# Performance work log

Hardware: AMD Instinct MI355X
Metric: run time of the kernel (lower is better)

The kernel has to match this reference:

```python
import jax, jax.numpy as jnp
import numpy as np

B, T, C, H = 2, 2048, 1024, 16
D = C // H  # head_dim = 64

def setup_inputs() -> dict:
    key = jax.random.key(0)
    k1, k2, k3, k4, k5 = jax.random.split(key, 5)
    x = jax.random.normal(k1, (B, T, C), dtype=jnp.float32)
    # RoPE tables (realistic frequencies)
    inv_freq = 1.0 / (10000.0 ** (jnp.arange(0, D // 2, dtype=jnp.float32) / (D // 2)))
    pos = jnp.arange(T, dtype=jnp.float32)
    ang = pos[:, None] * inv_freq[None, :]          # (T, D/2)
    cos, sin = jnp.cos(ang), jnp.sin(ang)
    # causal mask (True = keep)
    mask = jnp.tril(jnp.ones((T, T), dtype=bool))
    W_qkv = jax.random.normal(k2, (3 * C, C), dtype=jnp.float32) * (1.0 / np.sqrt(C))
    W_out = jax.random.normal(k3, (C, C), dtype=jnp.float32) * (1.0 / np.sqrt(C))
    return {"x": x, "cos": cos, "sin": sin, "mask": mask, "W_qkv": W_qkv, "W_out": W_out}

def apply_rope(x, cos, sin):
    # x: (B, H, T, D); cos/sin: (T, D/2)
    d = x.shape[-1] // 2
    x1, x2 = x[..., :d], x[..., d:]
    c = cos[None, None, :x.shape[2], :]
    s = sin[None, None, :x.shape[2], :]
    return jnp.concatenate([x1 * c - x2 * s, x2 * c + x1 * s], axis=-1)

def reference(x, cos, sin, mask, W_qkv, W_out):
    b, t, c = x.shape
    qkv = (x @ W_qkv.T).reshape(b, t, 3, H, D)
    q, k, v = qkv[:, :, 0], qkv[:, :, 1], qkv[:, :, 2]   # (b, t, H, D)
    q = q.transpose(0, 2, 1, 3)
    k = k.transpose(0, 2, 1, 3)
    v = v.transpose(0, 2, 1, 3)                           # (b, H, t, D)
    q = apply_rope(q, cos, sin)
    k = apply_rope(k, cos, sin)
    attn = jnp.einsum('bhqd,bhkd->bhqk', q, k) / jnp.sqrt(jnp.asarray(D, x.dtype))
    attn = jnp.where(mask[None, None, :, :], attn, -jnp.inf)
    attn = jax.nn.softmax(attn, axis=-1)
    out = jnp.einsum('bhqk,bhkd->bhqd', attn, v)          # (b, H, t, D)
    out = out.transpose(0, 2, 1, 3).reshape(b, t, c)
    return out @ W_out.T
```

## Files before the change

### kernel.cpp

```cpp
#include <hip/hip_runtime.h>
#include <stdint.h>

typedef __bf16 bf16;
typedef __bf16 bf16x4 __attribute__((ext_vector_type(4)));
typedef __bf16 bf16x8 __attribute__((ext_vector_type(8)));
typedef float f32x4 __attribute__((ext_vector_type(4)));

#define TSEQ 2048
#define NHEAD 16
#define HDIM 64
#define CDIM 1024

#define AS1(p) ((const __attribute__((address_space(1))) void*)(p))
#define AS3(p) ((__attribute__((address_space(3))) void*)(p))

#if __has_builtin(__builtin_amdgcn_exp2f)
#define EXP2(x) __builtin_amdgcn_exp2f(x)
#else
#define EXP2(x) exp2f(x)
#endif

__global__ __launch_bounds__(256) void cast3_bf16(const float* __restrict__ in1, int n1,
                                                  const float* __restrict__ in2, int n2,
                                                  const float* __restrict__ in3, int n3,
                                                  bf16* __restrict__ out1,
                                                  bf16* __restrict__ out2,
                                                  bf16* __restrict__ out3) {
  int i = (blockIdx.x * 256 + threadIdx.x) * 8;
  const float* src;
  bf16* dst;
  if (i < n1) {
    src = in1 + i; dst = out1 + i;
  } else if (i < n1 + n2) {
    src = in2 + (i - n1); dst = out2 + (i - n1);
  } else if (i < n1 + n2 + n3) {
    src = in3 + (i - n1 - n2); dst = out3 + (i - n1 - n2);
  } else {
    return;
  }
  float4 a = *(const float4*)src;
  float4 b = *(const float4*)(src + 4);
  bf16x8 r;
  r[0] = (bf16)a.x; r[1] = (bf16)a.y; r[2] = (bf16)a.z; r[3] = (bf16)a.w;
  r[4] = (bf16)b.x; r[5] = (bf16)b.y; r[6] = (bf16)b.z; r[7] = (bf16)b.w;
  *(bf16x8*)dst = r;
}

__global__ __launch_bounds__(256) void gemm_qkv_rope(const bf16* __restrict__ A,
                                                     const bf16* __restrict__ B,
                                                     const float* __restrict__ cosb,
                                                     const float* __restrict__ sinb,
                                                     bf16* __restrict__ Qb,
                                                     bf16* __restrict__ Kb,
                                                     bf16* __restrict__ Vt) {
  constexpr int K = 1024;
  __shared__ bf16 smem[8704];
  const int t = threadIdx.x;
  const int w = t >> 6, l = t & 63, g = l >> 4, ln = l & 15;
  const int wm = (w >> 1) * 64, wn = (w & 1) * 64;
  const int m0 = blockIdx.x * 128, n0 = blockIdx.y * 128;
  const int r0 = t >> 2, kc0 = (t & 3) * 8;

  f32x4 acc[4][4] = {};

  for (int k0 = 0; k0 < K; k0 += 32) {
    __syncthreads();
    __builtin_amdgcn_global_load_lds(AS1(A + (size_t)(m0 + r0) * K + k0 + kc0),
                                     AS3(&smem[t * 8]), 16, 0, 0);
    __builtin_amdgcn_global_load_lds(AS1(A + (size_t)(m0 + r0 + 64) * K + k0 + kc0),
                                     AS3(&smem[(t + 256) * 8]), 16, 0, 0);
    __builtin_amdgcn_global_load_lds(AS1(B + (size_t)(n0 + r0) * K + k0 + kc0),
                                     AS3(&smem[4096 + t * 8]), 16, 0, 0);
    __builtin_amdgcn_global_load_lds(AS1(B + (size_t)(n0 + r0 + 64) * K + k0 + kc0),
                                     AS3(&smem[4096 + (t + 256) * 8]), 16, 0, 0);
    __syncthreads();
    bf16x8 af[4], bfr[4];
#pragma unroll
    for (int i = 0; i < 4; i++) {
      af[i] = *(const bf16x8*)&smem[(wm + i * 16 + ln) * 32 + g * 8];
      bfr[i] = *(const bf16x8*)&smem[4096 + (wn + i * 16 + ln) * 32 + g * 8];
    }
#pragma unroll
    for (int i = 0; i < 4; i++)
#pragma unroll
      for (int j = 0; j < 4; j++)
        acc[i][j] = __builtin_amdgcn_mfma_f32_16x16x32_bf16(af[i], bfr[j], acc[i][j], 0, 0, 0);
  }

  const int part = n0 >> 10;
  if (part < 2) {
    bf16* dst = part ? Kb : Qb;
    const float qs = part ? 1.0f : 0.18033688011112042f;
#pragma unroll
    for (int i = 0; i < 4; i++)
#pragma unroll
      for (int j = 0; j < 2; j++) {
        int nl = (n0 & 1023) + wn + j * 16 + ln;
        int h = nl >> 6, d = nl & 31;
#pragma unroll
        for (int r = 0; r < 4; r++) {
          int row = m0 + wm + i * 16 + g * 4 + r;
          int tok = row & (TSEQ - 1), bb = row >> 11;
          float c = cosb[tok * 32 + d], s = sinb[tok * 32 + d];
          float a1 = acc[i][j][r], a2 = acc[i][j + 2][r];
          size_t ob = ((size_t)(bb * NHEAD + h) * TSEQ + tok) * HDIM + d;
          dst[ob] = (bf16)((a1 * c - a2 * s) * qs);
          dst[ob + 32] = (bf16)((a2 * c + a1 * s) * qs);
        }
      }
  } else {
    const int bb = m0 >> 11;
    const int tbase = m0 & (TSEQ - 1);
    const int nbase = n0 - 2048;
#pragma unroll
    for (int pass = 0; pass < 2; pass++) {
      __syncthreads();
      if ((w >> 1) == pass) {
#pragma unroll
        for (int i = 0; i < 4; i++)
#pragma unroll
          for (int j = 0; j < 4; j++) {
            int lr = i * 16 + g * 4;
            int lc = wn + j * 16 + ln;
#pragma unroll
            for (int r = 0; r < 4; r++)
              smem[(lr + r) * 132 + lc] = (bf16)acc[i][j][r];
          }
      }
      __syncthreads();
      for (int c = t; c < 1024; c += 256) {
        int ch = c >> 3, tc = c & 7;
        bf16x8 o;
#pragma unroll
        for (int j2 = 0; j2 < 8; j2++) o[j2] = smem[(tc * 8 + j2) * 132 + ch];
        int n = nbase + ch;
        int h = n >> 6, d = n & 63;
        *(bf16x8*)(Vt + ((size_t)((bb * NHEAD + h) * HDIM + d)) * TSEQ +
                   tbase + pass * 64 + tc * 8) = o;
      }
    }
  }
}

__global__ __launch_bounds__(256) void gemm_out(const bf16* __restrict__ A,
                                                const bf16* __restrict__ B,
                                                float* __restrict__ C,
                                                int M, int N, int K) {
  __shared__ bf16 As[64 * 32];
  __shared__ bf16 Bs[128 * 32];
  const int t = threadIdx.x;
  const int w = t >> 6, l = t & 63, g = l >> 4, ln = l & 15;
  const int m0 = blockIdx.x * 64, n0 = blockIdx.y * 128;
  const int r0 = t >> 2, kc0 = (t & 3) * 8;

  f32x4 acc[4][2] = {};

  for (int k0 = 0; k0 < K; k0 += 32) {
    __syncthreads();
    __builtin_amdgcn_global_load_lds(AS1(A + (size_t)(m0 + r0) * K + k0 + kc0),
                                     AS3(&As[t * 8]), 16, 0, 0);
    __builtin_amdgcn_global_load_lds(AS1(B + (size_t)(n0 + r0) * K + k0 + kc0),
                                     AS3(&Bs[t * 8]), 16, 0, 0);
    __builtin_amdgcn_global_load_lds(AS1(B + (size_t)(n0 + r0 + 64) * K + k0 + kc0),
                                     AS3(&Bs[(t + 256) * 8]), 16, 0, 0);
    __syncthreads();
    bf16x8 af[4], bfr[2];
#pragma unroll
    for (int i = 0; i < 4; i++)
      af[i] = *(const bf16x8*)&As[(i * 16 + ln) * 32 + g * 8];
#pragma unroll
    for (int j = 0; j < 2; j++)
      bfr[j] = *(const bf16x8*)&Bs[(w * 32 + j * 16 + ln) * 32 + g * 8];
#pragma unroll
    for (int i = 0; i < 4; i++)
#pragma unroll
      for (int j = 0; j < 2; j++)
        acc[i][j] = __builtin_amdgcn_mfma_f32_16x16x32_bf16(af[i], bfr[j], acc[i][j], 0, 0, 0);
  }
#pragma unroll
  for (int i = 0; i < 4; i++)
#pragma unroll
    for (int j = 0; j < 2; j++) {
      int row = m0 + i * 16 + g * 4;
      int col = n0 + w * 32 + j * 16 + ln;
#pragma unroll
      for (int r = 0; r < 4; r++)
        C[(size_t)(row + r) * N + col] = acc[i][j][r];
    }
}

__global__ __launch_bounds__(512) void attn_fwd(const bf16* __restrict__ Q,
                                                const bf16* __restrict__ K,
                                                const bf16* __restrict__ Vt,
                                                bf16* __restrict__ ctx) {
  __shared__ bf16 Ks[64 * 64];
  __shared__ bf16 VTs[64 * 64];
  __shared__ bf16 Ps[8][16 * 64];

  const int t = threadIdx.x;
  const int w = t >> 6;
  const int l = t & 63, g = l >> 4, ln = l & 15;
  const int bid = blockIdx.x;
  const int bh = bid & 31;
  const int qb0 = 15 - (bid >> 5);
  const size_t base = (size_t)bh * TSEQ * HDIM;

  const int q0 = qb0 * 128;
  const int qwb = q0 + w * 16;
  const int dtile = qwb >> 6;
  const int ktmax = 2 * qb0 + 1;
  const int q_global = qwb + ln;
  const int lswz = (ln & 7) * 8;

  const int r0 = t >> 3, ch0 = (t & 7) * 8;
  const int sidx = r0 * 64 + (((t & 7) ^ (r0 & 7)) * 8);

  bf16x8 bq[2];
  bq[0] = *(const bf16x8*)(Q + base + (size_t)q_global * HDIM + g * 8);
  bq[1] = *(const bf16x8*)(Q + base + (size_t)q_global * HDIM + 32 + g * 8);

  const bf16* kp = K + base + (size_t)r0 * HDIM + ch0;
  const bf16* vp = Vt + base + (size_t)r0 * TSEQ + ch0;
  bf16x8 kr = *(const bf16x8*)kp;
  bf16x8 vr = *(const bf16x8*)vp;

  f32x4 acc[4] = {};
  float l_run = 0.f;

  for (int kt = 0; kt <= ktmax; kt++) {
    __syncthreads();
    *(bf16x8*)&Ks[sidx] = kr;
    *(bf16x8*)&VTs[sidx] = vr;
    __syncthreads();
    if (kt < ktmax) {
      kr = *(const bf16x8*)(kp + (size_t)(kt + 1) * 64 * HDIM);
      vr = *(const bf16x8*)(vp + (kt + 1) * 64);
    }
    if (kt <= dtile) {
      f32x4 st[4] = {};
      __builtin_amdgcn_s_setprio(1);
#pragma unroll
      for (int step = 0; step < 2; step++)
#pragma unroll
        for (int mt = 0; mt < 4; mt++) {
          bf16x8 ak = *(const bf16x8*)&Ks[(mt * 16 + ln) * 64 + ((step * 32 + g * 8) ^ lswz)];
          st[mt] = __builtin_amdgcn_mfma_f32_16x16x32_bf16(ak, bq[step], st[mt], 0, 0, 0);
        }
      __builtin_amdgcn_s_setprio(0);
      float vals[16];
      if (kt == dtile) {
#pragma unroll
        for (int mt = 0; mt < 4; mt++)
#pragma unroll
          for (int r = 0; r < 4; r++) {
            int kg = kt * 64 + mt * 16 + g * 4 + r;
            vals[mt * 4 + r] = (kg <= q_global) ? fminf(st[mt][r], 60.f) : -INFINITY;
          }
      } else {
#pragma unroll
        for (int mt = 0; mt < 4; mt++)
#pragma unroll
          for (int r = 0; r < 4; r++) vals[mt * 4 + r] = fminf(st[mt][r], 60.f);
      }
      float psum = 0.f;
#pragma unroll
      for (int i2 = 0; i2 < 16; i2++) {
        float p = EXP2(vals[i2]);
        vals[i2] = p;
        psum += p;
      }
      psum += __shfl_xor(psum, 16);
      psum += __shfl_xor(psum, 32);
      l_run += psum;
#pragma unroll
      for (int mt = 0; mt < 4; mt++) {
        bf16x4 pk;
#pragma unroll
        for (int r = 0; r < 4; r++) pk[r] = (bf16)vals[mt * 4 + r];
        *(bf16x4*)&Ps[w][ln * 64 + (((mt * 16 + (g >> 1) * 8) ^ lswz) + (g & 1) * 4)] = pk;
      }
      __builtin_amdgcn_s_setprio(1);
#pragma unroll
      for (int step = 0; step < 2; step++) {
        bf16x8 ap = *(const bf16x8*)&Ps[w][ln * 64 + ((step * 32 + g * 8) ^ lswz)];
#pragma unroll
        for (int nt = 0; nt < 4; nt++) {
          bf16x8 bv = *(const bf16x8*)&VTs[(nt * 16 + ln) * 64 + ((step * 32 + g * 8) ^ lswz)];
          acc[nt] = __builtin_amdgcn_mfma_f32_16x16x32_bf16(ap, bv, acc[nt], 0, 0, 0);
        }
      }
      __builtin_amdgcn_s_setprio(0);
    }
  }

  float inv = 1.0f / l_run;
  float lrow[4];
#pragma unroll
  for (int r = 0; r < 4; r++) lrow[r] = __shfl(inv, g * 4 + r, 64);
  const int b = bh >> 4, h = bh & (NHEAD - 1);
#pragma unroll
  for (int nt = 0; nt < 4; nt++)
#pragma unroll
    for (int r = 0; r < 4; r++) {
      int q = qwb + g * 4 + r;
      ctx[(size_t)(b * TSEQ + q) * CDIM + h * HDIM + nt * 16 + ln] =
          (bf16)(acc[nt][r] * lrow[r]);
    }
}

extern "C" void kernel_launch(void* const* d_in, const int* in_sizes, int n_in,
                              void* d_out, int out_size, void* d_ws, size_t ws_size,
                              hipStream_t stream) {
  const float* x = (const float*)d_in[0];
  const float* cosb = (const float*)d_in[1];
  const float* sinb = (const float*)d_in[2];
  const float* Wqkv = (const float*)d_in[4];
  const float* Wout = (const float*)d_in[5];
  float* out = (float*)d_out;

  char* ws = (char*)d_ws;
  bf16* x_bf = (bf16*)ws;
  bf16* ctx = (bf16*)ws;
  bf16* Wqkv_bf = (bf16*)(ws + 8388608);
  bf16* Wout_bf = (bf16*)(ws + 14680064);
  bf16* Qb = (bf16*)(ws + 16777216);
  bf16* Kb = (bf16*)(ws + 25165824);
  bf16* Vt = (bf16*)(ws + 33554432);

  cast3_bf16<<<(4194304 + 3145728 + 1048576) / 8 / 256, 256, 0, stream>>>(
      x, 4194304, Wqkv, 3145728, Wout, 1048576, x_bf, Wqkv_bf, Wout_bf);
  gemm_qkv_rope<<<dim3(32, 24), 256, 0, stream>>>(x_bf, Wqkv_bf, cosb, sinb, Qb, Kb, Vt);
  attn_fwd<<<512, 512, 0, stream>>>(Qb, Kb, Vt, ctx);
  gemm_out<<<dim3(64, 8), 256, 0, stream>>>(ctx, Wout_bf, out, 4096, 1024, 1024);
}
```

Before: 184.8 us.

## Give each attention wave two query subtiles and double-buffer K/V tiles

The attention kernel now runs 4 waves of 32 query rows each instead of 8 waves of 16 rows. Each K fragment and each V fragment read from LDS is reused for two MFMAs, which halves LDS read traffic per matrix op. K/V LDS tiles are double-buffered so one __syncthreads per iteration goes away. The fminf(…,60) clamp on scores before exp2 is also dropped, which saves a few ALU ops but removes overflow protection. In exchange, each thread holds more accumulator registers and each block has fewer waves, which may lower latency hiding.

```diff
diff --git a/kernel.cpp b/kernel.cpp
--- a/kernel.cpp
+++ b/kernel.cpp
@@ -189,13 +189,13 @@
     }
 }
 
-__global__ __launch_bounds__(512) void attn_fwd(const bf16* __restrict__ Q,
+__global__ __launch_bounds__(256) void attn_fwd(const bf16* __restrict__ Q,
                                                 const bf16* __restrict__ K,
                                                 const bf16* __restrict__ Vt,
                                                 bf16* __restrict__ ctx) {
-  __shared__ bf16 Ks[64 * 64];
-  __shared__ bf16 VTs[64 * 64];
-  __shared__ bf16 Ps[8][16 * 64];
+  __shared__ bf16 Ks[2][64 * 64];
+  __shared__ bf16 VTs[2][64 * 64];
+  __shared__ bf16 Ps[4][2][16 * 64];
 
   const int t = threadIdx.x;
   const int w = t >> 6;
@@ -206,106 +206,130 @@
   const size_t base = (size_t)bh * TSEQ * HDIM;
 
   const int q0 = qb0 * 128;
-  const int qwb = q0 + w * 16;
+  const int qwb = q0 + w * 32;
   const int dtile = qwb >> 6;
   const int ktmax = 2 * qb0 + 1;
-  const int q_global = qwb + ln;
   const int lswz = (ln & 7) * 8;
 
   const int r0 = t >> 3, ch0 = (t & 7) * 8;
-  const int sidx = r0 * 64 + (((t & 7) ^ (r0 & 7)) * 8);
-
-  bf16x8 bq[2];
-  bq[0] = *(const bf16x8*)(Q + base + (size_t)q_global * HDIM + g * 8);
-  bq[1] = *(const bf16x8*)(Q + base + (size_t)q_global * HDIM + 32 + g * 8);
-
-  const bf16* kp = K + base + (size_t)r0 * HDIM + ch0;
-  const bf16* vp = Vt + base + (size_t)r0 * TSEQ + ch0;
-  bf16x8 kr = *(const bf16x8*)kp;
-  bf16x8 vr = *(const bf16x8*)vp;
-
-  f32x4 acc[4] = {};
-  float l_run = 0.f;
+  const int sx = ((t & 7) ^ (r0 & 7)) * 8;
+  const int s0 = r0 * 64 + sx;
+  const int s1 = (r0 + 32) * 64 + sx;
+
+  bf16x8 bq[2][2];
+#pragma unroll
+  for (int qs = 0; qs < 2; qs++) {
+    const int q_g = qwb + qs * 16 + ln;
+    bq[qs][0] = *(const bf16x8*)(Q + base + (size_t)q_g * HDIM + g * 8);
+    bq[qs][1] = *(const bf16x8*)(Q + base + (size_t)q_g * HDIM + 32 + g * 8);
+  }
+
+  const bf16* kp0 = K + base + (size_t)r0 * HDIM + ch0;
+  const bf16* kp1 = kp0 + 32 * HDIM;
+  const bf16* vp0 = Vt + base + (size_t)r0 * TSEQ + ch0;
+  const bf16* vp1 = vp0 + 32 * TSEQ;
+  bf16x8 kr0 = *(const bf16x8*)kp0;
+  bf16x8 kr1 = *(const bf16x8*)kp1;
+  bf16x8 vr0 = *(const bf16x8*)vp0;
+  bf16x8 vr1 = *(const bf16x8*)vp1;
+
+  f32x4 acc[2][4] = {};
+  float l_run[2] = {0.f, 0.f};
 
   for (int kt = 0; kt <= ktmax; kt++) {
-    __syncthreads();
-    *(bf16x8*)&Ks[sidx] = kr;
-    *(bf16x8*)&VTs[sidx] = vr;
+    bf16* ks = Ks[kt & 1];
+    bf16* vs = VTs[kt & 1];
+    *(bf16x8*)&ks[s0] = kr0;
+    *(bf16x8*)&ks[s1] = kr1;
+    *(bf16x8*)&vs[s0] = vr0;
+    *(bf16x8*)&vs[s1] = vr1;
     __syncthreads();
     if (kt < ktmax) {
-      kr = *(const bf16x8*)(kp + (size_t)(kt + 1) * 64 * HDIM);
-      vr = *(const bf16x8*)(vp + (kt + 1) * 64);
+      kr0 = *(const bf16x8*)(kp0 + (size_t)(kt + 1) * 64 * HDIM);
+      kr1 = *(const bf16x8*)(kp1 + (size_t)(kt + 1) * 64 * HDIM);
+      vr0 = *(const bf16x8*)(vp0 + (kt + 1) * 64);
+      vr1 = *(const bf16x8*)(vp1 + (kt + 1) * 64);
     }
     if (kt <= dtile) {
-      f32x4 st[4] = {};
+      f32x4 st[2][4] = {};
       __builtin_amdgcn_s_setprio(1);
 #pragma unroll
       for (int step = 0; step < 2; step++)
 #pragma unroll
         for (int mt = 0; mt < 4; mt++) {
-          bf16x8 ak = *(const bf16x8*)&Ks[(mt * 16 + ln) * 64 + ((step * 32 + g * 8) ^ lswz)];
-          st[mt] = __builtin_amdgcn_mfma_f32_16x16x32_bf16(ak, bq[step], st[mt], 0, 0, 0);
+          bf16x8 ak = *(const bf16x8*)&ks[(mt * 16 + ln) * 64 + ((step * 32 + g * 8) ^ lswz)];
+          st[0][mt] = __builtin_amdgcn_mfma_f32_16x16x32_bf16(ak, bq[0][step], st[0][mt], 0, 0, 0);
+          st[1][mt] = __builtin_amdgcn_mfma_f32_16x16x32_bf16(ak, bq[1][step], st[1][mt], 0, 0, 0);
         }
       __builtin_amdgcn_s_setprio(0);
-      float vals[16];
-      if (kt == dtile) {
-#pragma unroll
-        for (int mt = 0; mt < 4; mt++)
-#pragma unroll
-          for (int r = 0; r < 4; r++) {
-            int kg = kt * 64 + mt * 16 + g * 4 + r;
-            vals[mt * 4 + r] = (kg <= q_global) ? fminf(st[mt][r], 60.f) : -INFINITY;
-          }
-      } else {
-#pragma unroll
-        for (int mt = 0; mt < 4; mt++)
-#pragma unroll
-          for (int r = 0; r < 4; r++) vals[mt * 4 + r] = fminf(st[mt][r], 60.f);
-      }
-      float psum = 0.f;
-#pragma unroll
-      for (int i2 = 0; i2 < 16; i2++) {
-        float p = EXP2(vals[i2]);
-        vals[i2] = p;
-        psum += p;
-      }
-      psum += __shfl_xor(psum, 16);
-      psum += __shfl_xor(psum, 32);
-      l_run += psum;
-#pragma unroll
-      for (int mt = 0; mt < 4; mt++) {
-        bf16x4 pk;
-#pragma unroll
-        for (int r = 0; r < 4; r++) pk[r] = (bf16)vals[mt * 4 + r];
-        *(bf16x4*)&Ps[w][ln * 64 + (((mt * 16 + (g >> 1) * 8) ^ lswz) + (g & 1) * 4)] = pk;
+#pragma unroll
+      for (int qs2 = 0; qs2 < 2; qs2++) {
+        const int q_g = qwb + qs2 * 16 + ln;
+        float vals[16];
+        if (kt == dtile) {
+#pragma unroll
+          for (int mt = 0; mt < 4; mt++)
+#pragma unroll
+            for (int r = 0; r < 4; r++) {
+              int kg = kt * 64 + mt * 16 + g * 4 + r;
+              vals[mt * 4 + r] = (kg <= q_g) ? st[qs2][mt][r] : -INFINITY;
+            }
+        } else {
+#pragma unroll
+          for (int mt = 0; mt < 4; mt++)
+#pragma unroll
+            for (int r = 0; r < 4; r++) vals[mt * 4 + r] = st[qs2][mt][r];
+        }
+        float psum = 0.f;
+#pragma unroll
+        for (int i2 = 0; i2 < 16; i2++) {
+          float p = EXP2(vals[i2]);
+          vals[i2] = p;
+          psum += p;
+        }
+        psum += __shfl_xor(psum, 16);
+        psum += __shfl_xor(psum, 32);
+        l_run[qs2] += psum;
+#pragma unroll
+        for (int mt = 0; mt < 4; mt++) {
+          bf16x4 pk;
+#pragma unroll
+          for (int r = 0; r < 4; r++) pk[r] = (bf16)vals[mt * 4 + r];
+          *(bf16x4*)&Ps[w][qs2][ln * 64 + (((mt * 16 + (g >> 1) * 8) ^ lswz) + (g & 1) * 4)] = pk;
+        }
       }
       __builtin_amdgcn_s_setprio(1);
 #pragma unroll
       for (int step = 0; step < 2; step++) {
-        bf16x8 ap = *(const bf16x8*)&Ps[w][ln * 64 + ((step * 32 + g * 8) ^ lswz)];
+        bf16x8 ap0 = *(const bf16x8*)&Ps[w][0][ln * 64 + ((step * 32 + g * 8) ^ lswz)];
+        bf16x8 ap1 = *(const bf16x8*)&Ps[w][1][ln * 64 + ((step * 32 + g * 8) ^ lswz)];
 #pragma unroll
         for (int nt = 0; nt < 4; nt++) {
-          bf16x8 bv = *(const bf16x8*)&VTs[(nt * 16 + ln) * 64 + ((step * 32 + g * 8) ^ lswz)];
-          acc[nt] = __builtin_amdgcn_mfma_f32_16x16x32_bf16(ap, bv, acc[nt], 0, 0, 0);
+          bf16x8 bv = *(const bf16x8*)&vs[(nt * 16 + ln) * 64 + ((step * 32 + g * 8) ^ lswz)];
+          acc[0][nt] = __builtin_amdgcn_mfma_f32_16x16x32_bf16(ap0, bv, acc[0][nt], 0, 0, 0);
+          acc[1][nt] = __builtin_amdgcn_mfma_f32_16x16x32_bf16(ap1, bv, acc[1][nt], 0, 0, 0);
         }
       }
       __builtin_amdgcn_s_setprio(0);
     }
   }
 
-  float inv = 1.0f / l_run;
-  float lrow[4];
-#pragma unroll
-  for (int r = 0; r < 4; r++) lrow[r] = __shfl(inv, g * 4 + r, 64);
   const int b = bh >> 4, h = bh & (NHEAD - 1);
 #pragma unroll
-  for (int nt = 0; nt < 4; nt++)
-#pragma unroll
-    for (int r = 0; r < 4; r++) {
-      int q = qwb + g * 4 + r;
-      ctx[(size_t)(b * TSEQ + q) * CDIM + h * HDIM + nt * 16 + ln] =
-          (bf16)(acc[nt][r] * lrow[r]);
-    }
+  for (int qs2 = 0; qs2 < 2; qs2++) {
+    float inv = 1.0f / l_run[qs2];
+    float lrow[4];
+#pragma unroll
+    for (int r = 0; r < 4; r++) lrow[r] = __shfl(inv, g * 4 + r, 64);
+#pragma unroll
+    for (int nt = 0; nt < 4; nt++)
+#pragma unroll
+      for (int r = 0; r < 4; r++) {
+        int q = qwb + qs2 * 16 + g * 4 + r;
+        ctx[(size_t)(b * TSEQ + q) * CDIM + h * HDIM + nt * 16 + ln] =
+            (bf16)(acc[qs2][nt][r] * lrow[r]);
+      }
+  }
 }
 
 extern "C" void kernel_launch(void* const* d_in, const int* in_sizes, int n_in,
@@ -330,6 +354,6 @@
   cast3_bf16<<<(4194304 + 3145728 + 1048576) / 8 / 256, 256, 0, stream>>>(
       x, 4194304, Wqkv, 3145728, Wout, 1048576, x_bf, Wqkv_bf, Wout_bf);
   gemm_qkv_rope<<<dim3(32, 24), 256, 0, stream>>>(x_bf, Wqkv_bf, cosb, sinb, Qb, Kb, Vt);
-  attn_fwd<<<512, 512, 0, stream>>>(Qb, Kb, Vt, ctx);
+  attn_fwd<<<512, 256, 0, stream>>>(Qb, Kb, Vt, ctx);
   gemm_out<<<dim3(64, 8), 256, 0, stream>>>(ctx, Wout_bf, out, 4096, 1024, 1024);
 }
```

Result: slower. 196.3 us (+6.2%).

## Split attention KV range across two wave groups and merge partial results

Applied to the files above, without the earlier changes.

Doubles the attention block to 1024 threads, with two groups of 8 waves each processing alternate 64-key tiles. Each iteration now loads two K/V tiles. The partial accumulators and row sums are combined through shared memory at the end. The per-score clamp at 60 before exp2 is also removed. This raises in-block parallelism and halves the serial KV loop length per wave, at the cost of a larger shared-memory footprint, an extra reduction step and lower occupancy. Without the clamp, scores above 60 could overflow exp2 to infinity.

```diff
diff --git a/kernel.cpp b/kernel.cpp
--- a/kernel.cpp
+++ b/kernel.cpp
@@ -189,16 +189,21 @@
     }
 }
 
-__global__ __launch_bounds__(512) void attn_fwd(const bf16* __restrict__ Q,
-                                                const bf16* __restrict__ K,
-                                                const bf16* __restrict__ Vt,
-                                                bf16* __restrict__ ctx) {
-  __shared__ bf16 Ks[64 * 64];
-  __shared__ bf16 VTs[64 * 64];
-  __shared__ bf16 Ps[8][16 * 64];
+__global__ __launch_bounds__(1024, 8) void attn_fwd(const bf16* __restrict__ Q,
+                                                    const bf16* __restrict__ K,
+                                                    const bf16* __restrict__ Vt,
+                                                    bf16* __restrict__ ctx) {
+  __shared__ __align__(16) char smem_raw[65536];
+  bf16* Ks = (bf16*)smem_raw;
+  bf16* VTs = (bf16*)(smem_raw + 16384);
+  bf16* Ps = (bf16*)(smem_raw + 32768);
+  float* Mbuf = (float*)smem_raw;
+  float* Lbuf = (float*)(smem_raw + 32768);
 
   const int t = threadIdx.x;
   const int w = t >> 6;
+  const int p = w >> 3;
+  const int wq = w & 7;
   const int l = t & 63, g = l >> 4, ln = l & 15;
   const int bid = blockIdx.x;
   const int bh = bid & 31;
@@ -206,36 +211,38 @@
   const size_t base = (size_t)bh * TSEQ * HDIM;
 
   const int q0 = qb0 * 128;
-  const int qwb = q0 + w * 16;
+  const int qwb = q0 + wq * 16;
   const int dtile = qwb >> 6;
-  const int ktmax = 2 * qb0 + 1;
-  const int q_global = qwb + ln;
+  const int q_g = qwb + ln;
   const int lswz = (ln & 7) * 8;
 
-  const int r0 = t >> 3, ch0 = (t & 7) * 8;
-  const int sidx = r0 * 64 + (((t & 7) ^ (r0 & 7)) * 8);
+  const int ts = t >> 9;
+  const int tt = t & 511;
+  const int r0 = tt >> 3, ch0 = (tt & 7) * 8;
+  const int sidx = r0 * 64 + (((tt & 7) ^ (r0 & 7)) * 8);
 
   bf16x8 bq[2];
-  bq[0] = *(const bf16x8*)(Q + base + (size_t)q_global * HDIM + g * 8);
-  bq[1] = *(const bf16x8*)(Q + base + (size_t)q_global * HDIM + 32 + g * 8);
-
-  const bf16* kp = K + base + (size_t)r0 * HDIM + ch0;
-  const bf16* vp = Vt + base + (size_t)r0 * TSEQ + ch0;
+  bq[0] = *(const bf16x8*)(Q + base + (size_t)q_g * HDIM + g * 8);
+  bq[1] = *(const bf16x8*)(Q + base + (size_t)q_g * HDIM + 32 + g * 8);
+
+  const bf16* kp = K + base + (size_t)(ts * 64 + r0) * HDIM + ch0;
+  const bf16* vp = Vt + base + (size_t)r0 * TSEQ + ts * 64 + ch0;
   bf16x8 kr = *(const bf16x8*)kp;
   bf16x8 vr = *(const bf16x8*)vp;
 
   f32x4 acc[4] = {};
   float l_run = 0.f;
 
-  for (int kt = 0; kt <= ktmax; kt++) {
-    __syncthreads();
-    *(bf16x8*)&Ks[sidx] = kr;
-    *(bf16x8*)&VTs[sidx] = vr;
-    __syncthreads();
-    if (kt < ktmax) {
-      kr = *(const bf16x8*)(kp + (size_t)(kt + 1) * 64 * HDIM);
-      vr = *(const bf16x8*)(vp + (kt + 1) * 64);
-    }
+  for (int i = 0; i <= qb0; i++) {
+    __syncthreads();
+    *(bf16x8*)&Ks[ts * 4096 + sidx] = kr;
+    *(bf16x8*)&VTs[ts * 4096 + sidx] = vr;
+    __syncthreads();
+    if (i < qb0) {
+      kr = *(const bf16x8*)(kp + (size_t)(i + 1) * 128 * HDIM);
+      vr = *(const bf16x8*)(vp + (i + 1) * 128);
+    }
+    const int kt = 2 * i + p;
     if (kt <= dtile) {
       f32x4 st[4] = {};
       __builtin_amdgcn_s_setprio(1);
@@ -243,7 +250,8 @@
       for (int step = 0; step < 2; step++)
 #pragma unroll
         for (int mt = 0; mt < 4; mt++) {
-          bf16x8 ak = *(const bf16x8*)&Ks[(mt * 16 + ln) * 64 + ((step * 32 + g * 8) ^ lswz)];
+          bf16x8 ak = *(const bf16x8*)&Ks[p * 4096 + (mt * 16 + ln) * 64 +
+                                          ((step * 32 + g * 8) ^ lswz)];
           st[mt] = __builtin_amdgcn_mfma_f32_16x16x32_bf16(ak, bq[step], st[mt], 0, 0, 0);
         }
       __builtin_amdgcn_s_setprio(0);
@@ -254,20 +262,20 @@
 #pragma unroll
           for (int r = 0; r < 4; r++) {
             int kg = kt * 64 + mt * 16 + g * 4 + r;
-            vals[mt * 4 + r] = (kg <= q_global) ? fminf(st[mt][r], 60.f) : -INFINITY;
+            vals[mt * 4 + r] = (kg <= q_g) ? st[mt][r] : -INFINITY;
           }
       } else {
 #pragma unroll
         for (int mt = 0; mt < 4; mt++)
 #pragma unroll
-          for (int r = 0; r < 4; r++) vals[mt * 4 + r] = fminf(st[mt][r], 60.f);
+          for (int r = 0; r < 4; r++) vals[mt * 4 + r] = st[mt][r];
       }
       float psum = 0.f;
 #pragma unroll
       for (int i2 = 0; i2 < 16; i2++) {
-        float p = EXP2(vals[i2]);
-        vals[i2] = p;
-        psum += p;
+        float pv = EXP2(vals[i2]);
+        vals[i2] = pv;
+        psum += pv;
       }
       psum += __shfl_xor(psum, 16);
       psum += __shfl_xor(psum, 32);
@@ -277,15 +285,17 @@
         bf16x4 pk;
 #pragma unroll
         for (int r = 0; r < 4; r++) pk[r] = (bf16)vals[mt * 4 + r];
-        *(bf16x4*)&Ps[w][ln * 64 + (((mt * 16 + (g >> 1) * 8) ^ lswz) + (g & 1) * 4)] = pk;
+        *(bf16x4*)&Ps[w * 1024 + ln * 64 +
+                      (((mt * 16 + (g >> 1) * 8) ^ lswz) + (g & 1) * 4)] = pk;
       }
       __builtin_amdgcn_s_setprio(1);
 #pragma unroll
       for (int step = 0; step < 2; step++) {
-        bf16x8 ap = *(const bf16x8*)&Ps[w][ln * 64 + ((step * 32 + g * 8) ^ lswz)];
+        bf16x8 ap = *(const bf16x8*)&Ps[w * 1024 + ln * 64 + ((step * 32 + g * 8) ^ lswz)];
 #pragma unroll
         for (int nt = 0; nt < 4; nt++) {
-          bf16x8 bv = *(const bf16x8*)&VTs[(nt * 16 + ln) * 64 + ((step * 32 + g * 8) ^ lswz)];
+          bf16x8 bv = *(const bf16x8*)&VTs[p * 4096 + (nt * 16 + ln) * 64 +
+                                           ((step * 32 + g * 8) ^ lswz)];
           acc[nt] = __builtin_amdgcn_mfma_f32_16x16x32_bf16(ap, bv, acc[nt], 0, 0, 0);
         }
       }
@@ -293,19 +303,32 @@
     }
   }
 
-  float inv = 1.0f / l_run;
-  float lrow[4];
-#pragma unroll
-  for (int r = 0; r < 4; r++) lrow[r] = __shfl(inv, g * 4 + r, 64);
-  const int b = bh >> 4, h = bh & (NHEAD - 1);
-#pragma unroll
-  for (int nt = 0; nt < 4; nt++)
-#pragma unroll
-    for (int r = 0; r < 4; r++) {
-      int q = qwb + g * 4 + r;
-      ctx[(size_t)(b * TSEQ + q) * CDIM + h * HDIM + nt * 16 + ln] =
-          (bf16)(acc[nt][r] * lrow[r]);
-    }
+  __syncthreads();
+  if (p == 1) {
+#pragma unroll
+    for (int nt = 0; nt < 4; nt++)
+      *(f32x4*)&Mbuf[(wq * 64 + l) * 16 + nt * 4] = acc[nt];
+    Lbuf[wq * 64 + l] = l_run;
+  }
+  __syncthreads();
+  if (p == 0) {
+#pragma unroll
+    for (int nt = 0; nt < 4; nt++) acc[nt] += *(const f32x4*)&Mbuf[(wq * 64 + l) * 16 + nt * 4];
+    l_run += Lbuf[wq * 64 + l];
+    float inv = 1.0f / l_run;
+    float lrow[4];
+#pragma unroll
+    for (int r = 0; r < 4; r++) lrow[r] = __shfl(inv, g * 4 + r, 64);
+    const int b = bh >> 4, h = bh & (NHEAD - 1);
+#pragma unroll
+    for (int nt = 0; nt < 4; nt++)
+#pragma unroll
+      for (int r = 0; r < 4; r++) {
+        int q = qwb + g * 4 + r;
+        ctx[(size_t)(b * TSEQ + q) * CDIM + h * HDIM + nt * 16 + ln] =
+            (bf16)(acc[nt][r] * lrow[r]);
+      }
+  }
 }
 
 extern "C" void kernel_launch(void* const* d_in, const int* in_sizes, int n_in,
@@ -330,6 +353,6 @@
   cast3_bf16<<<(4194304 + 3145728 + 1048576) / 8 / 256, 256, 0, stream>>>(
       x, 4194304, Wqkv, 3145728, Wout, 1048576, x_bf, Wqkv_bf, Wout_bf);
   gemm_qkv_rope<<<dim3(32, 24), 256, 0, stream>>>(x_bf, Wqkv_bf, cosb, sinb, Qb, Kb, Vt);
-  attn_fwd<<<512, 512, 0, stream>>>(Qb, Kb, Vt, ctx);
+  attn_fwd<<<512, 1024, 0, stream>>>(Qb, Kb, Vt, ctx);
   gemm_out<<<dim3(64, 8), 256, 0, stream>>>(ctx, Wout_bf, out, 4096, 1024, 1024);
 }
```

New measurement: 193.2 us. 4.6% more time.
